# Kernel tuning notes

Measured on AMD Instinct MI355X. Metric: run time of the kernel, lower is better.

Reference implementation:

```python
import jax, jax.numpy as jnp
import numpy as np
from jax import lax

B, N, C = 16, 1024, 768
HID = 128           # route_hidden_dim (Cattn bottleneck + router hidden)
OUT = 2304          # qkv out_feature


def setup_inputs() -> dict:
    key = jax.random.key(0)
    ks = jax.random.split(key, 16)
    s = 0.02
    return {
        "input":  jax.random.normal(ks[0], (B, N, C), jnp.float32),
        "H": 32,
        "W": 32,
        "input2": jax.random.normal(ks[1], (B, N, C), jnp.float32),
        # qkv linear
        "qkv_w": jax.random.normal(ks[2], (OUT, C), jnp.float32) * s,
        "qkv_b": jax.random.normal(ks[3], (OUT,), jnp.float32) * s,
        # Cattn (vida_refine): fc1 -> dwconv -> gelu -> fc2
        "fc1_w": jax.random.normal(ks[4], (HID, C), jnp.float32) * s,
        "fc1_b": jnp.zeros((HID,), jnp.float32),
        "dw_w":  jax.random.normal(ks[5], (HID, 1, 3, 3), jnp.float32) * np.sqrt(2.0 / 9.0),
        "dw_b":  jnp.zeros((HID,), jnp.float32),
        "fc2_w": jax.random.normal(ks[6], (C, HID), jnp.float32) * s,
        "fc2_b": jnp.zeros((C,), jnp.float32),
        # router MLP: 1 -> HID -> 2
        "r1_w": jax.random.normal(ks[7], (HID, 1), jnp.float32) * s,
        "r1_b": jnp.zeros((HID,), jnp.float32),
        "r2_w": jax.random.normal(ks[8], (2, HID), jnp.float32) * s,
        "r2_b": jnp.zeros((2,), jnp.float32),
    }


def _linear(x, w, b):
    return jnp.einsum("bnc,oc->bno", x, w) + b


def _cattn(x, H, W, fc1_w, fc1_b, dw_w, dw_b, fc2_w, fc2_b):
    # fc1 -> depthwise 3x3 conv over HxW -> GELU(exact) -> fc2
    x = _linear(x, fc1_w, fc1_b)                       # [B,N,HID]
    b, n, h = x.shape
    xi = x.transpose(0, 2, 1).reshape(b, h, H, W)      # [B,HID,H,W]
    xi = lax.conv_general_dilated(
        xi, dw_w, window_strides=(1, 1), padding="SAME",
        feature_group_count=h,
        dimension_numbers=("NCHW", "OIHW", "NCHW"),
    ) + dw_b[None, :, None, None]
    x = xi.reshape(b, h, n).transpose(0, 2, 1)         # [B,N,HID]
    x = jax.nn.gelu(x, approximate=False)              # torch nn.GELU default = erf
    return _linear(x, fc2_w, fc2_b)                    # [B,N,C]


def _get_logit(inp, refine_x2):
    # cosine sim between per-batch token-mean of `inp` and refine_x2, then
    # per-batch min-max normalization (skipped when max == min)
    mean = jnp.mean(inp, axis=1, keepdims=True)        # [B,1,C]
    dot = jnp.sum(refine_x2 * mean, axis=-1, keepdims=True)
    n1 = jnp.linalg.norm(mean, axis=-1, keepdims=True)
    n2 = jnp.linalg.norm(refine_x2, axis=-1, keepdims=True)
    csim = dot / (n1 * n2)                             # [B,N,1]
    mn = jnp.min(csim, axis=1, keepdims=True)
    mx = jnp.max(csim, axis=1, keepdims=True)
    rng = mx - mn
    return jnp.where(rng != 0, (csim - mn) / jnp.where(rng != 0, rng, 1.0), csim)


def reference(input, H, W, input2, qkv_w, qkv_b, fc1_w, fc1_b, dw_w, dw_b,
              fc2_w, fc2_b, r1_w, r1_b, r2_w, r2_b):
    q1 = _linear(input, qkv_w, qkv_b)                              # [B,N,OUT]
    refine_x2 = input2 + _cattn(input2, H, W, fc1_w, fc1_b, dw_w, dw_b, fc2_w, fc2_b)
    q2 = _linear(refine_x2, qkv_w, qkv_b)                          # [B,N,OUT]
    csim = _get_logit(input, refine_x2)                            # [B,N,1]
    h = jax.nn.relu(_linear(csim, r1_w, r1_b))                     # [B,N,HID]
    logits = jax.nn.sigmoid(_linear(h, r2_w, r2_b))                # [B,N,2]
    # gumbel_softmax(hard=False, tau=1) with a fixed key for determinism
    g = jax.random.gumbel(jax.random.key(42), logits.shape, logits.dtype)
    router = jax.nn.softmax(logits + g, axis=-1)[:, :, 0]          # [B,N]
    return (q1, q2, router)
```

## Files before the change

### kernel.cpp

```cpp
#include <hip/hip_runtime.h>
#include <cstdint>
#include <cstddef>

#define BQ 16
#define NT 1024
#define CH 768
#define HIDN 128
#define OUTF 2304
#define MTOT (BQ*NT)

typedef __attribute__((ext_vector_type(4))) float f32x4;
typedef __attribute__((ext_vector_type(8))) short short8;

__device__ __forceinline__ unsigned short f2bf(float f){
  unsigned u = __float_as_uint(f);
  u += 0x7FFFu + ((u >> 16) & 1u);
  return (unsigned short)(u >> 16);
}
__device__ __forceinline__ float bf2f(unsigned short h){
  return __uint_as_float(((unsigned)h) << 16);
}

__device__ __forceinline__ void gload16(const void* g, void* l){
  __builtin_amdgcn_global_load_lds((const __attribute__((address_space(1))) void*)g,
                                   (__attribute__((address_space(3))) void*)l, 16, 0, 0);
}

__device__ __forceinline__ void mfma16(f32x4& d, short8 a, short8 b){
  asm volatile("v_mfma_f32_16x16x32_bf16 %0, %1, %2, %0" : "+v"(d) : "v"(a), "v"(b));
}

__device__ __forceinline__ short8 pack8(float4 a, float4 b){
  short8 p;
  p[0]=(short)f2bf(a.x); p[1]=(short)f2bf(a.y); p[2]=(short)f2bf(a.z); p[3]=(short)f2bf(a.w);
  p[4]=(short)f2bf(b.x); p[5]=(short)f2bf(b.y); p[6]=(short)f2bf(b.z); p[7]=(short)f2bf(b.w);
  return p;
}

#define STAGE(matB_, buf_, h_, t_) { \
    const unsigned short* g_ = ((matB_) ? Bbase : Abase) + (size_t)(h_)*128*K + (size_t)(t_)*64; \
    char* d_ = ldsWaveDst + (matB_)*65536 + (buf_)*32768 + (h_)*16384; \
    gload16(g_, d_); \
    gload16(g_ + rowK64, d_ + 8192); \
  }

#define PH_OPEN() \
    asm volatile("s_barrier" ::: "memory"); \
    asm volatile("s_waitcnt lgkmcnt(0)" ::: "memory"); \
    __builtin_amdgcn_sched_barrier(0); \
    __builtin_amdgcn_s_setprio(1);

#define PH_CLOSE() \
    __builtin_amdgcn_s_setprio(0); \
    asm volatile("s_barrier" ::: "memory");

#define MF16(mb, nb, BV) \
    _Pragma("unroll") \
    for (int ks = 0; ks < 2; ++ks) \
      _Pragma("unroll") \
      for (int mf = 0; mf < 4; ++mf) \
        _Pragma("unroll") \
        for (int nf = 0; nf < 2; ++nf) \
          mfma16(acc[(mb)+mf][(nb)+nf], av[mf][ks], BV[nf][ks]);

#define TILE(t_, b_) { \
    const int t = (t_); const int b = (b_); \
    _Pragma("unroll") for (int mf = 0; mf < 4; ++mf){ av[mf][0]=ldA(b,mf,0); av[mf][1]=ldA(b,mf,1); } \
    _Pragma("unroll") for (int nf = 0; nf < 2; ++nf){ b0v[nf][0]=ldB(b,nf,0); b0v[nf][1]=ldB(b,nf,1); } \
    if (t+1 < T) STAGE(0, b^1, 1, t+1); \
    PH_OPEN(); MF16(0,0,b0v); PH_CLOSE(); \
    _Pragma("unroll") for (int nf = 0; nf < 2; ++nf){ b1v[nf][0]=ldB(b,2+nf,0); b1v[nf][1]=ldB(b,2+nf,1); } \
    if (t+1 < T) STAGE(1, b^1, 0, t+1); \
    PH_OPEN(); MF16(0,2,b1v); PH_CLOSE(); \
    _Pragma("unroll") for (int mf = 0; mf < 4; ++mf){ av[mf][0]=ldA(b,4+mf,0); av[mf][1]=ldA(b,4+mf,1); } \
    if (t+2 < T) STAGE(0, b, 0, t+2); \
    PH_OPEN(); MF16(4,2,b1v); PH_CLOSE(); \
    if (t+2 < T) STAGE(1, b, 1, t+2); \
    PH_OPEN(); MF16(4,0,b0v); \
    __builtin_amdgcn_s_setprio(0); \
    if (t+2 < T) { asm volatile("s_waitcnt vmcnt(4)" ::: "memory"); } \
    else         { asm volatile("s_waitcnt vmcnt(0)" ::: "memory"); } \
    asm volatile("s_barrier" ::: "memory"); \
  }

template<int T>
__device__ __forceinline__
void gemm256_body(char* lds8,
                  const unsigned short* __restrict__ A,
                  const unsigned short* __restrict__ B,
                  const float* __restrict__ bias,
                  float* __restrict__ C,
                  int N, int K, int nbn, int bid, int nwg)
{
  const int tid = threadIdx.x;
  const int ln = tid & 63, wv = tid >> 6;
  const int wm = wv >> 2, wn = wv & 3;
  const int llo = ln & 15, lhi = ln >> 4;

  const int cpx = nwg >> 3;
  const int swz = (bid & 7) * cpx + (bid >> 3);
  const int bm = swz / nbn, bn = swz % nbn;
  const int m0 = bm * 256, n0 = bn * 256;

  const int srow = tid >> 3;
  const int sslot = (tid & 7) ^ (srow & 7);
  const unsigned short* Abase = A + (size_t)(m0 + srow) * K + sslot * 8;
  const unsigned short* Bbase = B + (size_t)(n0 + srow) * K + sslot * 8;
  const size_t rowK64 = (size_t)64 * K;
  char* ldsWaveDst = lds8 + (wv << 10);

  const int swz0 = ((lhi ^ (ln & 7)) << 4);
  const char* aRd0 = lds8 + (wm*64 + llo)*128 + swz0;
  const char* aRd1 = lds8 + (wm*64 + llo)*128 + (swz0 ^ 64);
  const char* bRd0 = lds8 + 65536 + (wn*32 + llo)*128 + swz0;
  const char* bRd1 = lds8 + 65536 + (wn*32 + llo)*128 + (swz0 ^ 64);

  auto ldA = [&](int b, int mf, int ks) -> short8 {
    const char* p = (ks ? aRd1 : aRd0) + b*32768 + (mf>>2)*16384 + (mf&3)*2048;
    return *reinterpret_cast<const short8*>(p);
  };
  auto ldB = [&](int b, int nf, int ks) -> short8 {
    const char* p = (ks ? bRd1 : bRd0) + b*32768 + (nf>>1)*16384 + (nf&1)*2048;
    return *reinterpret_cast<const short8*>(p);
  };

  f32x4 acc[8][4];
  #pragma unroll
  for (int m = 0; m < 8; ++m)
    #pragma unroll
    for (int n = 0; n < 4; ++n) acc[m][n] = 0.0f;

  STAGE(0, 0, 0, 0);
  STAGE(1, 0, 1, 0);
  STAGE(0, 0, 1, 0);
  STAGE(1, 0, 0, 0);
  STAGE(0, 1, 0, 1);
  STAGE(1, 1, 1, 1);
  asm volatile("s_waitcnt vmcnt(4)" ::: "memory");
  asm volatile("s_barrier" ::: "memory");

  short8 av[4][2], b0v[2][2], b1v[2][2];
  #pragma unroll 1
  for (int t0 = 0; t0 < T; t0 += 2){
    TILE(t0,   0);
    TILE(t0+1, 1);
  }

  asm volatile("s_nop 7\n\ts_nop 7\n\ts_nop 7" ::: );

  #pragma unroll
  for (int mf = 0; mf < 8; ++mf){
    const int row = m0 + (mf>>2)*128 + wm*64 + (mf&3)*16 + lhi*4;
    #pragma unroll
    for (int j = 0; j < 4; ++j){
      #pragma unroll
      for (int nf = 0; nf < 4; ++nf){
        const int col = n0 + (nf>>1)*128 + wn*32 + (nf&1)*16 + llo;
        C[(size_t)(row + j) * N + col] = acc[mf][nf][j] + bias[col];
      }
    }
  }
}

__device__ __forceinline__
void fc1f32_body(char* lds, const float* __restrict__ A, const float* __restrict__ B,
                 const float* __restrict__ bias, unsigned short* __restrict__ Cb, int fb)
{
  unsigned short (*sA)[32] = (unsigned short(*)[32])lds;
  unsigned short (*sB)[32] = (unsigned short(*)[32])(lds + 8192);
  const int tid = threadIdx.x;
  const int wv = tid >> 6, ln = tid & 63;
  const int wr = wv >> 1, wc = wv & 1;
  const int lhi = ln >> 4, llo = ln & 15;
  const int m0 = fb * 128;
  const int N = 128;
  const int srow = tid >> 1, scol = (tid & 1) * 16;
  const float* Ap = A + (size_t)(m0 + srow) * 768 + scol;
  const float* Bp = B + (size_t)srow * 768 + scol;

  f32x4 acc[4][4];
  #pragma unroll
  for (int m = 0; m < 4; ++m)
    #pragma unroll
    for (int n = 0; n < 4; ++n) acc[m][n] = 0.0f;

  #pragma unroll 1
  for (int kt = 0; kt < 768; kt += 32){
    float4 a4[4], b4[4];
    #pragma unroll
    for (int j = 0; j < 4; ++j){
      a4[j] = *reinterpret_cast<const float4*>(Ap + kt + j*4);
      b4[j] = *reinterpret_cast<const float4*>(Bp + kt + j*4);
    }
    *reinterpret_cast<short8*>(&sA[srow][scol])     = pack8(a4[0], a4[1]);
    *reinterpret_cast<short8*>(&sA[srow][scol + 8]) = pack8(a4[2], a4[3]);
    *reinterpret_cast<short8*>(&sB[srow][scol])     = pack8(b4[0], b4[1]);
    *reinterpret_cast<short8*>(&sB[srow][scol + 8]) = pack8(b4[2], b4[3]);
    __syncthreads();

    short8 av[4], bv[4];
    #pragma unroll
    for (int m = 0; m < 4; ++m)
      av[m] = *reinterpret_cast<const short8*>(&sA[wr*64 + m*16 + llo][lhi*8]);
    #pragma unroll
    for (int n = 0; n < 4; ++n)
      bv[n] = *reinterpret_cast<const short8*>(&sB[wc*64 + n*16 + llo][lhi*8]);

    #pragma unroll
    for (int m = 0; m < 4; ++m)
      #pragma unroll
      for (int n = 0; n < 4; ++n)
        mfma16(acc[m][n], bv[n], av[m]);
    __syncthreads();
  }

  asm volatile("s_nop 7\n\ts_nop 7\n\ts_nop 7" ::: );

  float4 bias4[4];
  #pragma unroll
  for (int n = 0; n < 4; ++n)
    bias4[n] = *reinterpret_cast<const float4*>(&bias[wc*64 + n*16 + lhi*4]);

  #pragma unroll
  for (int m = 0; m < 4; ++m){
    const int row = m0 + wr*64 + m*16 + llo;
    #pragma unroll
    for (int n = 0; n < 4; ++n){
      const int colbase = wc*64 + n*16 + lhi*4;
      ushort4 o;
      o.x = f2bf(acc[m][n][0] + bias4[n].x);
      o.y = f2bf(acc[m][n][1] + bias4[n].y);
      o.z = f2bf(acc[m][n][2] + bias4[n].z);
      o.w = f2bf(acc[m][n][3] + bias4[n].w);
      *reinterpret_cast<ushort4*>(&Cb[(size_t)row * N + colbase]) = o;
    }
  }
}

__device__ __forceinline__
void meanf32_body(char* lds, const float* __restrict__ input,
                  float* __restrict__ meanb, float* __restrict__ n1p, int mbid)
{
  float (*tmp)[128] = (float(*)[128])lds;
  const int b = mbid / 6, cg = mbid % 6;
  const int tid = threadIdx.x;
  const int oct = tid & 15, rg = tid >> 4;
  const float* ip = input + (size_t)b*NT*CH + (size_t)rg*64*CH + cg*128 + oct*8;

  float s[8];
  #pragma unroll
  for (int j = 0; j < 8; ++j) s[j] = 0.f;
  #pragma unroll 2
  for (int r = 0; r < 64; ++r){
    float4 v0 = *reinterpret_cast<const float4*>(ip + (size_t)r*CH);
    float4 v1 = *reinterpret_cast<const float4*>(ip + (size_t)r*CH + 4);
    s[0]+=v0.x; s[1]+=v0.y; s[2]+=v0.z; s[3]+=v0.w;
    s[4]+=v1.x; s[5]+=v1.y; s[6]+=v1.z; s[7]+=v1.w;
  }
  #pragma unroll
  for (int j = 0; j < 8; ++j) tmp[rg][oct*8 + j] = s[j];
  __syncthreads();

  if (tid < 128){
    float m = 0.f;
    #pragma unroll
    for (int g = 0; g < 16; ++g) m += tmp[g][tid];
    m *= (1.0f/1024.0f);
    meanb[b*CH + cg*128 + tid] = m;
    float q = m * m;
    for (int off = 32; off; off >>= 1) q += __shfl_down(q, off, 64);
    if ((tid & 63) == 0) n1p[b*12 + cg*2 + (tid >> 6)] = q;
  }
}

__global__ void k_mega(const float* __restrict__ input, const float* __restrict__ input2,
                       const float* __restrict__ qkv_w, const float* __restrict__ fc2_w,
                       unsigned short* __restrict__ x1b, unsigned short* __restrict__ xrb,
                       unsigned short* __restrict__ wqb, unsigned short* __restrict__ w2b,
                       const float* __restrict__ fc1_w, const float* __restrict__ fc1_b,
                       unsigned short* __restrict__ t1dst,
                       float* __restrict__ meanb, float* __restrict__ n1p)
{
  __shared__ __align__(64) char lds[16384];
  const int bid = blockIdx.x;
  if (bid < 128){
    fc1f32_body(lds, input2, fc1_w, fc1_b, t1dst, bid);
  } else if (bid < 224){
    meanf32_body(lds, input, meanb, n1p, bid - 128);
  } else {
    const long step = (long)2048 * 256 * 4;
    for (long i = (long)((bid - 224) * 256 + threadIdx.x) * 4; i < 27033600L; i += step){
      const float* s; unsigned short* d; long off;
      if      (i < 12582912L){ s = input;  d = x1b; off = i; }
      else if (i < 25165824L){ s = input2; d = xrb; off = i - 12582912L; }
      else if (i < 26935296L){ s = qkv_w;  d = wqb; off = i - 25165824L; }
      else                   { s = fc2_w;  d = w2b; off = i - 26935296L; }
      float4 v = *reinterpret_cast<const float4*>(s + off);
      ushort4 o;
      o.x = f2bf(v.x); o.y = f2bf(v.y); o.z = f2bf(v.z); o.w = f2bf(v.w);
      *reinterpret_cast<ushort4*>(d + off) = o;
    }
  }
}

__device__ __forceinline__ void threefry(unsigned k0, unsigned k1, unsigned x0, unsigned x1,
                                         unsigned& o0, unsigned& o1){
  unsigned ks2 = k0 ^ k1 ^ 0x1BD11BDAu;
  x0 += k0; x1 += k1;
#define TFR(r) { x0 += x1; x1 = (x1 << r) | (x1 >> (32 - r)); x1 ^= x0; }
  TFR(13) TFR(15) TFR(26) TFR(6)  x0 += k1;  x1 += ks2 + 1u;
  TFR(17) TFR(29) TFR(16) TFR(24) x0 += ks2; x1 += k0 + 2u;
  TFR(13) TFR(15) TFR(26) TFR(6)  x0 += k0;  x1 += k1 + 3u;
  TFR(17) TFR(29) TFR(16) TFR(24) x0 += k1;  x1 += ks2 + 4u;
  TFR(13) TFR(15) TFR(26) TFR(6)  x0 += ks2; x1 += k0 + 5u;
#undef TFR
  o0 = x0; o1 = x1;
}

__device__ __forceinline__ float gumbel_from_bits(unsigned bits){
  float f = __uint_as_float((bits >> 9) | 0x3F800000u) - 1.0f;
  const float TINY = 1.17549435e-38f;
  float u = fmaxf(TINY, f + TINY);
  return -logf(-logf(u));
}

__device__ __forceinline__
void router_body(char* lds, const float* __restrict__ part, const float* __restrict__ n1p,
                 const float* __restrict__ r1w, const float* __restrict__ r1b,
                 const float* __restrict__ r2w, const float* __restrict__ r2b,
                 float* __restrict__ out, int b)
{
  float* cs   = (float*)lds;
  float* red  = (float*)(lds + 4096);
  float* w1s  = (float*)(lds + 4096 + 64);
  float* b1s  = w1s + HIDN;
  float* w20s = b1s + HIDN;
  float* w21s = w20s + HIDN;
  const int tid = threadIdx.x;
  if (tid < HIDN){
    w1s[tid]  = r1w[tid];
    b1s[tid]  = r1b[tid];
    w20s[tid] = r2w[tid];
    w21s[tid] = r2w[HIDN + tid];
  }
  float n1s = 0.f;
  #pragma unroll
  for (int s = 0; s < 12; ++s) n1s += n1p[b*12 + s];
  float n1 = sqrtf(n1s);
  float lmin = 3.4e38f, lmax = -3.4e38f;
  #pragma unroll
  for (int j = 0; j < 2; ++j){
    int tk = tid + j*512;
    int t = b*NT + tk;
    float dot = 0.f, q = 0.f;
    #pragma unroll
    for (int s = 0; s < 12; ++s){
      dot += part[(size_t)s * MTOT + t];
      q   += part[(size_t)(12 + s) * MTOT + t];
    }
    float v = dot / (n1 * sqrtf(q));
    cs[tk] = v;
    lmin = fminf(lmin, v); lmax = fmaxf(lmax, v);
  }
  int ln = tid & 63, wv = tid >> 6;
  for (int off = 32; off; off >>= 1){
    lmin = fminf(lmin, __shfl_down(lmin, off, 64));
    lmax = fmaxf(lmax, __shfl_down(lmax, off, 64));
  }
  if (ln == 0){ red[wv] = lmin; red[8+wv] = lmax; }
  __syncthreads();
  float mn = red[0], mx = red[8];
  #pragma unroll
  for (int s = 1; s < 8; ++s){ mn = fminf(mn, red[s]); mx = fmaxf(mx, red[8+s]); }
  float rng = mx - mn;
  bool nz = (rng != 0.0f);

  const float r2b0 = r2b[0], r2b1 = r2b[1];
  float v[2], l0[2], l1[2];
  #pragma unroll
  for (int j = 0; j < 2; ++j){
    float c0 = cs[tid + j*512];
    v[j] = nz ? (c0 - mn) / rng : c0;
    l0[j] = r2b0; l1[j] = r2b1;
  }
  for (int k = 0; k < HIDN; ++k){
    float a = w1s[k], bb = b1s[k], c0 = w20s[k], c1 = w21s[k];
    #pragma unroll
    for (int j = 0; j < 2; ++j){
      float hh = fmaxf(v[j] * a + bb, 0.f);
      l0[j] += hh * c0;
      l1[j] += hh * c1;
    }
  }
  #pragma unroll
  for (int j = 0; j < 2; ++j){
    float s0 = 1.f / (1.f + expf(-l0[j]));
    float s1 = 1.f / (1.f + expf(-l1[j]));
    int t = b*NT + tid + j*512;
    unsigned o0, o1;
    threefry(0u, 42u, 0u, (unsigned)(2*t),     o0, o1);
    float g0 = gumbel_from_bits(o0 ^ o1);
    threefry(0u, 42u, 0u, (unsigned)(2*t + 1), o0, o1);
    float g1 = gumbel_from_bits(o0 ^ o1);
    out[t] = 1.f / (1.f + expf((s1 + g1) - (s0 + g0)));
  }
}

__global__ __launch_bounds__(512, 2)
void k_combo2(const unsigned short* __restrict__ Aall, const unsigned short* __restrict__ wqb,
              const float* __restrict__ qkv_b, float* __restrict__ q1q2,
              const float* __restrict__ part, const float* __restrict__ n1p,
              const float* __restrict__ r1w, const float* __restrict__ r1b,
              const float* __restrict__ r2w, const float* __restrict__ r2b,
              float* __restrict__ router)
{
  __shared__ __align__(1024) char lds8[131072];
  const int bid = blockIdx.x;
  if (bid < 1152){
    gemm256_body<CH/64>(lds8, Aall, wqb, qkv_b, q1q2, OUTF, CH, OUTF/256, bid, 1152);
  } else {
    router_body(lds8, part, n1p, r1w, r1b, r2w, r2b, router, bid - 1152);
  }
}

__global__ __launch_bounds__(256, 2)
void k_gemm_fc2(const unsigned short* __restrict__ A, const unsigned short* __restrict__ B,
                const float* __restrict__ bias, const unsigned short* __restrict__ addb,
                unsigned short* __restrict__ Cb,
                const float* __restrict__ meanb, float* __restrict__ part,
                int M, int N, int K)
{
  __shared__ unsigned short sA[128][32];
  __shared__ unsigned short sB[128][32];
  const int tid = threadIdx.x;
  const int wv = tid >> 6, ln = tid & 63;
  const int wr = wv >> 1, wc = wv & 1;
  const int lhi = ln >> 4, llo = ln & 15;
  const int m0 = blockIdx.x * 128, n0 = blockIdx.y * 128;

  f32x4 acc[4][4];
  #pragma unroll
  for (int m = 0; m < 4; ++m)
    #pragma unroll
    for (int n = 0; n < 4; ++n) acc[m][n] = 0.0f;

  const int lrow = ln >> 2;
  const int lk8  = (ln & 3) * 8;

  for (int kt = 0; kt < K; kt += 32){
    #pragma unroll
    for (int cc = 0; cc < 2; ++cc){
      int c = wv * 2 + cc;
      gload16(A + (size_t)(m0 + c*16 + lrow) * K + kt + lk8, &sA[c*16][0]);
      gload16(B + (size_t)(n0 + c*16 + lrow) * K + kt + lk8, &sB[c*16][0]);
    }
    __syncthreads();

    short8 av[4], bv[4];
    #pragma unroll
    for (int m = 0; m < 4; ++m)
      av[m] = *reinterpret_cast<const short8*>(&sA[wr*64 + m*16 + llo][lhi*8]);
    #pragma unroll
    for (int n = 0; n < 4; ++n)
      bv[n] = *reinterpret_cast<const short8*>(&sB[wc*64 + n*16 + llo][lhi*8]);

    #pragma unroll
    for (int m = 0; m < 4; ++m)
      #pragma unroll
      for (int n = 0; n < 4; ++n)
        mfma16(acc[m][n], bv[n], av[m]);
    __syncthreads();
  }

  asm volatile("s_nop 7\n\ts_nop 7\n\ts_nop 7" ::: );

  float4 bias4[4];
  #pragma unroll
  for (int n = 0; n < 4; ++n)
    bias4[n] = *reinterpret_cast<const float4*>(&bias[n0 + wc*64 + n*16 + lhi*4]);

  const int bb = m0 >> 10;
  const float* mp = meanb + bb * CH;
  float4 mp4[4];
  #pragma unroll
  for (int n = 0; n < 4; ++n)
    mp4[n] = *reinterpret_cast<const float4*>(&mp[n0 + wc*64 + n*16 + lhi*4]);

  #pragma unroll
  for (int m = 0; m < 4; ++m){
    const int row = m0 + wr*64 + m*16 + llo;
    float dsum = 0.f, qsum = 0.f;
    #pragma unroll
    for (int n = 0; n < 4; ++n){
      const int colbase = n0 + wc*64 + n*16 + lhi*4;
      ushort4 a4 = *reinterpret_cast<const ushort4*>(&addb[(size_t)row * N + colbase]);
      float v0 = acc[m][n][0] + bias4[n].x + bf2f(a4.x);
      float v1 = acc[m][n][1] + bias4[n].y + bf2f(a4.y);
      float v2 = acc[m][n][2] + bias4[n].z + bf2f(a4.z);
      float v3 = acc[m][n][3] + bias4[n].w + bf2f(a4.w);
      ushort4 o; o.x = f2bf(v0); o.y = f2bf(v1); o.z = f2bf(v2); o.w = f2bf(v3);
      *reinterpret_cast<ushort4*>(&Cb[(size_t)row * N + colbase]) = o;
      dsum += v0*mp4[n].x + v1*mp4[n].y + v2*mp4[n].z + v3*mp4[n].w;
      qsum += v0*v0 + v1*v1 + v2*v2 + v3*v3;
    }
    dsum += __shfl_xor(dsum, 16, 64);  qsum += __shfl_xor(qsum, 16, 64);
    dsum += __shfl_xor(dsum, 32, 64);  qsum += __shfl_xor(qsum, 32, 64);
    if (ln < 16){
      const int slot = blockIdx.y * 2 + wc;
      part[(size_t)slot * MTOT + row] = dsum;
      part[(size_t)(12 + slot) * MTOT + row] = qsum;
    }
  }
}

__global__ void k_dwgelu(const unsigned short* __restrict__ t1b, const float* __restrict__ dww,
                         const float* __restrict__ dwb, unsigned short* __restrict__ t2)
{
  int idx = blockIdx.x * blockDim.x + threadIdx.x;
  int hq = idx & 31; int t = idx >> 5;
  int h = hq * 4;
  int n = t & (NT-1); int b = t >> 10;
  int y = n >> 5, x = n & 31;

  float w[4][9];
  #pragma unroll
  for (int i = 0; i < 4; ++i)
    #pragma unroll
    for (int k = 0; k < 9; ++k) w[i][k] = dww[(h+i)*9 + k];

  float a0 = dwb[h+0], a1 = dwb[h+1], a2 = dwb[h+2], a3 = dwb[h+3];
  #pragma unroll
  for (int dy = -1; dy <= 1; ++dy){
    int yy = y + dy; if ((unsigned)yy >= 32u) continue;
    #pragma unroll
    for (int dx = -1; dx <= 1; ++dx){
      int xx = x + dx; if ((unsigned)xx >= 32u) continue;
      ushort4 v = *reinterpret_cast<const ushort4*>(&t1b[((size_t)b*NT + yy*32 + xx)*HIDN + h]);
      int k = (dy+1)*3 + (dx+1);
      a0 += bf2f(v.x) * w[0][k]; a1 += bf2f(v.y) * w[1][k];
      a2 += bf2f(v.z) * w[2][k]; a3 += bf2f(v.w) * w[3][k];
    }
  }
  const float is2 = 0.70710678118654752440f;
  a0 = 0.5f*a0*(1.0f + erff(a0*is2));
  a1 = 0.5f*a1*(1.0f + erff(a1*is2));
  a2 = 0.5f*a2*(1.0f + erff(a2*is2));
  a3 = 0.5f*a3*(1.0f + erff(a3*is2));
  ushort4 o; o.x = f2bf(a0); o.y = f2bf(a1); o.z = f2bf(a2); o.w = f2bf(a3);
  *reinterpret_cast<ushort4*>(&t2[(size_t)t*HIDN + h]) = o;
}

extern "C" void kernel_launch(void* const* d_in, const int* in_sizes, int n_in,
                              void* d_out, int out_size, void* d_ws, size_t ws_size,
                              hipStream_t stream)
{
  (void)in_sizes; (void)n_in; (void)out_size;
  const float* input  = (const float*)d_in[0];
  const float* input2 = (const float*)d_in[3];
  const float* qkv_w  = (const float*)d_in[4];
  const float* qkv_b  = (const float*)d_in[5];
  const float* fc1_w  = (const float*)d_in[6];
  const float* fc1_b  = (const float*)d_in[7];
  const float* dw_w   = (const float*)d_in[8];
  const float* dw_b   = (const float*)d_in[9];
  const float* fc2_w  = (const float*)d_in[10];
  const float* fc2_b  = (const float*)d_in[11];
  const float* r1_w   = (const float*)d_in[12];
  const float* r1_b   = (const float*)d_in[13];
  const float* r2_w   = (const float*)d_in[14];
  const float* r2_b   = (const float*)d_in[15];

  float* q1 = (float*)d_out;
  float* router = q1 + (size_t)2 * MTOT * OUTF;

  if (ws_size < 67000000u) return;

  char* ws = (char*)d_ws;
  unsigned short* x1b = (unsigned short*)ws; ws += (size_t)MTOT*CH*2;
  unsigned short* xrb = (unsigned short*)ws; ws += (size_t)MTOT*CH*2;
  unsigned short* wqb = (unsigned short*)ws; ws += (size_t)OUTF*CH*2;
  ws += (size_t)HIDN*CH*2;
  unsigned short* w2b = (unsigned short*)ws; ws += (size_t)CH*HIDN*2;
  unsigned short* t1b = (unsigned short*)ws; ws += (size_t)MTOT*HIDN*4;
  unsigned short* t2  = (unsigned short*)ws; ws += (size_t)MTOT*HIDN*2;
  float*          mb  = (float*)ws;          ws += (size_t)BQ*CH*4;
  float*          n1p = (float*)ws;          ws += 1024;
  float*          part= (float*)t1b;

  unsigned short* t1dst = t1b + (size_t)MTOT*HIDN;
  k_mega<<<dim3(2272), 256, 0, stream>>>(
      input, input2, qkv_w, fc2_w, x1b, xrb, wqb, w2b,
      fc1_w, fc1_b, t1dst, mb, n1p);

  k_dwgelu<<<dim3(MTOT*32/256), 256, 0, stream>>>(t1dst, dw_w, dw_b, t2);

  k_gemm_fc2<<<dim3(MTOT/128, CH/128), 256, 0, stream>>>(
      t2, w2b, fc2_b, xrb, xrb, mb, part, MTOT, CH, HIDN);

  k_combo2<<<dim3(1168), 512, 0, stream>>>(
      x1b, wqb, qkv_b, q1, part, n1p, r1_w, r1_b, r2_w, r2_b, router);
}
```

Before: 233.7 us.

## Fuse depthwise conv and GELU into fc2 GEMM A-tile producer

```diff
diff --git a/kernel.cpp b/kernel.cpp
--- a/kernel.cpp
+++ b/kernel.cpp
@@ -424,20 +424,33 @@
 }
 
 __global__ __launch_bounds__(256, 2)
-void k_gemm_fc2(const unsigned short* __restrict__ A, const unsigned short* __restrict__ B,
-                const float* __restrict__ bias, const unsigned short* __restrict__ addb,
-                unsigned short* __restrict__ Cb,
-                const float* __restrict__ meanb, float* __restrict__ part,
-                int M, int N, int K)
+void k_gemm_fc2f(const unsigned short* __restrict__ t1, const unsigned short* __restrict__ B,
+                 const float* __restrict__ dww, const float* __restrict__ dwb,
+                 const float* __restrict__ bias, const unsigned short* __restrict__ addb,
+                 unsigned short* __restrict__ Cb,
+                 const float* __restrict__ meanb, float* __restrict__ part,
+                 int M, int N, int K)
 {
   __shared__ unsigned short sA[128][32];
   __shared__ unsigned short sB[128][32];
+  __shared__ float wt[9][128];
+  __shared__ float bdw[128];
   const int tid = threadIdx.x;
+  for (int i = tid; i < 1152; i += 256){ int c = i / 9; int k = i - c*9; wt[k][c] = dww[i]; }
+  if (tid < 128) bdw[tid] = dwb[tid];
+
   const int wv = tid >> 6, ln = tid & 63;
   const int wr = wv >> 1, wc = wv & 1;
   const int lhi = ln >> 4, llo = ln & 15;
   const int m0 = blockIdx.x * 128, n0 = blockIdx.y * 128;
 
+  const int srow = tid >> 1;
+  const int posc = (tid & 1) * 16;
+  const int tok = m0 + srow;
+  const int bimg = tok >> 10, nn = tok & 1023;
+  const int y = nn >> 5, x = nn & 31;
+  const unsigned short* t1base = t1 + (((size_t)bimg << 10)) * HIDN;
+
   f32x4 acc[4][4];
   #pragma unroll
   for (int m = 0; m < 4; ++m)
@@ -447,13 +460,50 @@
   const int lrow = ln >> 2;
   const int lk8  = (ln & 3) * 8;
 
-  for (int kt = 0; kt < K; kt += 32){
+  __syncthreads();
+
+  #pragma unroll 1
+  for (int kt = 0; kt < 128; kt += 32){
     #pragma unroll
     for (int cc = 0; cc < 2; ++cc){
       int c = wv * 2 + cc;
-      gload16(A + (size_t)(m0 + c*16 + lrow) * K + kt + lk8, &sA[c*16][0]);
       gload16(B + (size_t)(n0 + c*16 + lrow) * K + kt + lk8, &sB[c*16][0]);
     }
+    const int c0 = kt + posc;
+    float a[16];
+    #pragma unroll
+    for (int j = 0; j < 16; ++j) a[j] = bdw[c0 + j];
+    #pragma unroll
+    for (int dy = -1; dy <= 1; ++dy){
+      int yy = y + dy; if ((unsigned)yy >= 32u) continue;
+      #pragma unroll
+      for (int dx = -1; dx <= 1; ++dx){
+        int xx = x + dx; if ((unsigned)xx >= 32u) continue;
+        const unsigned short* src = t1base + (size_t)(yy*32 + xx) * HIDN + c0;
+        short8 v0 = *reinterpret_cast<const short8*>(src);
+        short8 v1 = *reinterpret_cast<const short8*>(src + 8);
+        const int k = (dy+1)*3 + (dx+1);
+        const float* wk = &wt[k][c0];
+        #pragma unroll
+        for (int j = 0; j < 8; ++j) a[j]     += bf2f((unsigned short)v0[j]) * wk[j];
+        #pragma unroll
+        for (int j = 0; j < 8; ++j) a[8 + j] += bf2f((unsigned short)v1[j]) * wk[8 + j];
+      }
+    }
+    const float is2 = 0.70710678118654752440f;
+    short8 g0, g1;
+    #pragma unroll
+    for (int j = 0; j < 8; ++j){
+      float t = a[j];
+      g0[j] = (short)f2bf(0.5f * t * (1.0f + erff(t * is2)));
+    }
+    #pragma unroll
+    for (int j = 0; j < 8; ++j){
+      float t = a[8 + j];
+      g1[j] = (short)f2bf(0.5f * t * (1.0f + erff(t * is2)));
+    }
+    *reinterpret_cast<short8*>(&sA[srow][posc])     = g0;
+    *reinterpret_cast<short8*>(&sA[srow][posc + 8]) = g1;
     __syncthreads();
 
     short8 av[4], bv[4];
@@ -511,43 +561,6 @@
       part[(size_t)(12 + slot) * MTOT + row] = qsum;
     }
   }
-}
-
-__global__ void k_dwgelu(const unsigned short* __restrict__ t1b, const float* __restrict__ dww,
-                         const float* __restrict__ dwb, unsigned short* __restrict__ t2)
-{
-  int idx = blockIdx.x * blockDim.x + threadIdx.x;
-  int hq = idx & 31; int t = idx >> 5;
-  int h = hq * 4;
-  int n = t & (NT-1); int b = t >> 10;
-  int y = n >> 5, x = n & 31;
-
-  float w[4][9];
-  #pragma unroll
-  for (int i = 0; i < 4; ++i)
-    #pragma unroll
-    for (int k = 0; k < 9; ++k) w[i][k] = dww[(h+i)*9 + k];
-
-  float a0 = dwb[h+0], a1 = dwb[h+1], a2 = dwb[h+2], a3 = dwb[h+3];
-  #pragma unroll
-  for (int dy = -1; dy <= 1; ++dy){
-    int yy = y + dy; if ((unsigned)yy >= 32u) continue;
-    #pragma unroll
-    for (int dx = -1; dx <= 1; ++dx){
-      int xx = x + dx; if ((unsigned)xx >= 32u) continue;
-      ushort4 v = *reinterpret_cast<const ushort4*>(&t1b[((size_t)b*NT + yy*32 + xx)*HIDN + h]);
-      int k = (dy+1)*3 + (dx+1);
-      a0 += bf2f(v.x) * w[0][k]; a1 += bf2f(v.y) * w[1][k];
-      a2 += bf2f(v.z) * w[2][k]; a3 += bf2f(v.w) * w[3][k];
-    }
-  }
-  const float is2 = 0.70710678118654752440f;
-  a0 = 0.5f*a0*(1.0f + erff(a0*is2));
-  a1 = 0.5f*a1*(1.0f + erff(a1*is2));
-  a2 = 0.5f*a2*(1.0f + erff(a2*is2));
-  a3 = 0.5f*a3*(1.0f + erff(a3*is2));
-  ushort4 o; o.x = f2bf(a0); o.y = f2bf(a1); o.z = f2bf(a2); o.w = f2bf(a3);
-  *reinterpret_cast<ushort4*>(&t2[(size_t)t*HIDN + h]) = o;
 }
 
 extern "C" void kernel_launch(void* const* d_in, const int* in_sizes, int n_in,
@@ -582,7 +595,7 @@
   ws += (size_t)HIDN*CH*2;
   unsigned short* w2b = (unsigned short*)ws; ws += (size_t)CH*HIDN*2;
   unsigned short* t1b = (unsigned short*)ws; ws += (size_t)MTOT*HIDN*4;
-  unsigned short* t2  = (unsigned short*)ws; ws += (size_t)MTOT*HIDN*2;
+  ws += (size_t)MTOT*HIDN*2;
   float*          mb  = (float*)ws;          ws += (size_t)BQ*CH*4;
   float*          n1p = (float*)ws;          ws += 1024;
   float*          part= (float*)t1b;
@@ -592,10 +605,8 @@
       input, input2, qkv_w, fc2_w, x1b, xrb, wqb, w2b,
       fc1_w, fc1_b, t1dst, mb, n1p);
 
-  k_dwgelu<<<dim3(MTOT*32/256), 256, 0, stream>>>(t1dst, dw_w, dw_b, t2);
-
-  k_gemm_fc2<<<dim3(MTOT/128, CH/128), 256, 0, stream>>>(
-      t2, w2b, fc2_b, xrb, xrb, mb, part, MTOT, CH, HIDN);
+  k_gemm_fc2f<<<dim3(MTOT/128, CH/128), 256, 0, stream>>>(
+      t1dst, w2b, dw_w, dw_b, fc2_b, xrb, xrb, mb, part, MTOT, CH, HIDN);
 
   k_combo2<<<dim3(1168), 512, 0, stream>>>(
       x1b, wqb, qkv_b, q1, part, n1p, r1_w, r1_b, r2_w, r2_b, router);
```

New measurement: 239.9 us. +2.7%, slower.
